# Kernel tuning notes

Measured on AMD Instinct MI355X. Metric: run time of the kernel, lower is better.

The kernel has to match this reference:

```python
import jax, jax.numpy as jnp
import numpy as np

DIM = 1024
NUM_HEADS = 16
HEAD_DIM = DIM // NUM_HEADS
BINDING_BIAS = 0.5
SCALE = HEAD_DIM ** -0.5


def setup_inputs() -> dict:
    key = jax.random.key(0)
    ks = jax.random.split(key, 10)
    B, S, D = 2, 2048, DIM
    std = D ** -0.5
    return {
        "x": jax.random.normal(ks[0], (B, S, D), jnp.float32),
        "binding_matrix": jax.random.uniform(ks[1], (S, S), jnp.float32),
        "Wq": jax.random.normal(ks[2], (D, D), jnp.float32) * std,
        "bq": jnp.zeros((D,), jnp.float32),
        "Wk": jax.random.normal(ks[3], (D, D), jnp.float32) * std,
        "bk": jnp.zeros((D,), jnp.float32),
        "Wv": jax.random.normal(ks[4], (D, D), jnp.float32) * std,
        "bv": jnp.zeros((D,), jnp.float32),
        "Wo": jax.random.normal(ks[5], (D, D), jnp.float32) * std,
        "bo": jnp.zeros((D,), jnp.float32),
    }


def reference(x, binding_matrix, Wq, bq, Wk, bk, Wv, bv, Wo, bo):
    B, S, D = x.shape
    H, Hd = NUM_HEADS, HEAD_DIM
    # projections -> [B, H, S, Hd]
    q = (x @ Wq + bq).reshape(B, S, H, Hd).transpose(0, 2, 1, 3)
    k = (x @ Wk + bk).reshape(B, S, H, Hd).transpose(0, 2, 1, 3)
    v = (x @ Wv + bv).reshape(B, S, H, Hd).transpose(0, 2, 1, 3)
    # scores [B, H, S, S] with additive binding bias
    attn = jnp.einsum("bhqd,bhkd->bhqk", q, k) * SCALE
    attn = attn + BINDING_BIAS * binding_matrix[None, None, :, :]
    attn = jax.nn.softmax(attn, axis=-1)
    out = jnp.einsum("bhqk,bhkd->bhqd", attn, v)
    out = out.transpose(0, 2, 1, 3).reshape(B, S, D)
    return out @ Wo + bo
```

## Files before the change

### kernel.cpp

```cpp
#include <hip/hip_runtime.h>

#define DEV static __device__ __forceinline__

typedef __attribute__((ext_vector_type(4))) float f32x4;
typedef __attribute__((ext_vector_type(8))) __bf16 bfv8;
typedef __attribute__((ext_vector_type(8))) short s8v;
typedef __attribute__((ext_vector_type(4))) short s4v;

DEV short f2bf(float f) {
    unsigned u = __float_as_uint(f);
    u = (u + 0x7fffu + ((u >> 16) & 1u)) >> 16;
    return (short)u;
}
DEV float bf2f(short s) { return __uint_as_float(((unsigned)(unsigned short)s) << 16); }

DEV void gload16(const void* g, void* l) {
    __builtin_amdgcn_global_load_lds(
        (const __attribute__((address_space(1))) void*)g,
        (__attribute__((address_space(3))) void*)l, 16, 0, 0);
}

DEV f32x4 mfma16(bfv8 a, bfv8 b, f32x4 c) {
    return __builtin_amdgcn_mfma_f32_16x16x32_bf16(a, b, c, 0, 0, 0);
}

DEV float max3f(float a, float b, float c) {
    float d;
    asm("v_max3_f32 %0, %1, %2, %3" : "=v"(d) : "v"(a), "v"(b), "v"(c));
    return d;
}

DEV bfv8 ldsfrag(const short* base, int row, int slog) {
    int sp = slog ^ (row & 7);
    return *reinterpret_cast<const bfv8*>(base + row * 64 + sp * 8);
}

__global__ void k_cvt(const float* __restrict__ in, short* __restrict__ out, float s) {
    int i = blockIdx.x * blockDim.x + threadIdx.x;
    const float4* p = (const float4*)in + (size_t)i * 2;
    float4 a = p[0], b = p[1];
    s8v o;
    o[0] = f2bf(a.x * s); o[1] = f2bf(a.y * s); o[2] = f2bf(a.z * s); o[3] = f2bf(a.w * s);
    o[4] = f2bf(b.x * s); o[5] = f2bf(b.y * s); o[6] = f2bf(b.z * s); o[7] = f2bf(b.w * s);
    reinterpret_cast<s8v*>(out)[i] = o;
}

__global__ void k_transpose4(
    const float* __restrict__ W0, const float* __restrict__ W1,
    const float* __restrict__ W2, const float* __restrict__ W3,
    short* __restrict__ T0, short* __restrict__ T1,
    short* __restrict__ T2, short* __restrict__ T3, float s0)
{
    __shared__ float tl[32][33];
    const int z = blockIdx.z;
    const float* W = z == 0 ? W0 : z == 1 ? W1 : z == 2 ? W2 : W3;
    short* Wt = z == 0 ? T0 : z == 1 ? T1 : z == 2 ? T2 : T3;
    const float s = z == 0 ? s0 : 1.f;
    int tx = threadIdx.x & 31, ty = threadIdx.x >> 5;
    int nb = blockIdx.x * 32, kb = blockIdx.y * 32;
#pragma unroll
    for (int i = 0; i < 4; i++)
        tl[ty + i * 8][tx] = W[(kb + ty + i * 8) * 1024 + nb + tx];
    __syncthreads();
#pragma unroll
    for (int i = 0; i < 4; i++)
        Wt[(nb + ty + i * 8) * 1024 + kb + tx] = f2bf(tl[tx][ty + i * 8] * s);
}

template <int EPI>
DEV void gemm_body(const short* __restrict__ A, const short* __restrict__ Bt,
                   const float* __restrict__ bias, void* __restrict__ outp,
                   float bscale, int row0, int col0, short* As, short* Bs)
{
    const int t = threadIdx.x, lane = t & 63;
    const int wv = t >> 6, wr = wv >> 1, wc = wv & 1;
    const int g = lane >> 4, c = lane & 15;

    const f32x4 z4 = {0.f, 0.f, 0.f, 0.f};
    f32x4 acc[2][4];
#pragma unroll
    for (int m = 0; m < 2; m++)
#pragma unroll
        for (int n = 0; n < 4; n++) acc[m][n] = z4;

    for (int kt = 0; kt < 16; ++kt) {
        const int k0 = kt * 64;
        const short* Ag = A + row0 * 1024 + k0;
        const short* Bg = Bt + col0 * 1024 + k0;
#pragma unroll
        for (int j = 0; j < 2; j++) {
            int idx = j * 256 + t;
            int row = idx >> 3, sp = idx & 7, sl = sp ^ (row & 7);
            gload16(Ag + row * 1024 + sl * 8, As + idx * 8);
        }
#pragma unroll
        for (int j = 0; j < 4; j++) {
            int idx = j * 256 + t;
            int row = idx >> 3, sp = idx & 7, sl = sp ^ (row & 7);
            gload16(Bg + row * 1024 + sl * 8, Bs + idx * 8);
        }
        __syncthreads();

        bfv8 af[2][2], bfr[4][2];
#pragma unroll
        for (int m = 0; m < 2; m++)
#pragma unroll
            for (int ks = 0; ks < 2; ks++)
                af[m][ks] = ldsfrag(As, wr * 32 + m * 16 + c, ks * 4 + g);
#pragma unroll
        for (int n = 0; n < 4; n++)
#pragma unroll
            for (int ks = 0; ks < 2; ks++)
                bfr[n][ks] = ldsfrag(Bs, wc * 64 + n * 16 + c, ks * 4 + g);
        __builtin_amdgcn_s_setprio(1);
#pragma unroll
        for (int m = 0; m < 2; m++)
#pragma unroll
            for (int n = 0; n < 4; n++)
#pragma unroll
                for (int ks = 0; ks < 2; ks++)
                    acc[m][n] = mfma16(af[m][ks], bfr[n][ks], acc[m][n]);
        __builtin_amdgcn_s_setprio(0);
        __syncthreads();
    }

#pragma unroll
    for (int n = 0; n < 4; n++) {
        const int gc = col0 + wc * 64 + n * 16 + c;
        const float bvl = bias[gc] * bscale;
        const int h = gc >> 6, d = gc & 63;
#pragma unroll
        for (int m = 0; m < 2; m++) {
            const int gr = row0 + wr * 32 + m * 16 + g * 4;
            if (EPI == 2) {
                float* O = (float*)outp;
#pragma unroll
                for (int r = 0; r < 4; r++) O[(gr + r) * 1024 + gc] = acc[m][n][r] + bvl;
            } else {
                const int b = gr >> 11, sr = gr & 2047;
                short* O = (short*)outp;
                if (EPI == 0) {
                    int base = ((b * 16 + h) * 2048 + sr) * 64 + d;
#pragma unroll
                    for (int r = 0; r < 4; r++) O[base + r * 64] = f2bf(acc[m][n][r] + bvl);
                } else {
                    s4v vv;
#pragma unroll
                    for (int r = 0; r < 4; r++) vv[r] = f2bf(acc[m][n][r] + bvl);
                    *reinterpret_cast<s4v*>(O + ((b * 16 + h) * 64 + d) * 2048 + sr) = vv;
                }
            }
        }
    }
}

__global__ __launch_bounds__(256, 2) void k_gemm3(
    const short* __restrict__ A,
    const short* __restrict__ WqT, const short* __restrict__ WkT, const short* __restrict__ WvT,
    const float* __restrict__ bq, const float* __restrict__ bk, const float* __restrict__ bv,
    short* __restrict__ Qs, short* __restrict__ Kst, short* __restrict__ Vts, float scq)
{
    __shared__ alignas(16) short As[64 * 64];
    __shared__ alignas(16) short Bs[128 * 64];
    const int which = blockIdx.y >> 3;
    const int col0 = (blockIdx.y & 7) * 128;
    const int row0 = blockIdx.x * 64;
    if (which == 0)
        gemm_body<0>(A, WqT, bq, Qs, scq, row0, col0, As, Bs);
    else if (which == 1)
        gemm_body<0>(A, WkT, bk, Kst, 1.f, row0, col0, As, Bs);
    else
        gemm_body<1>(A, WvT, bv, Vts, 1.f, row0, col0, As, Bs);
}

__global__ __launch_bounds__(256, 2) void k_gemmO(
    const short* __restrict__ A, const short* __restrict__ Bt,
    const float* __restrict__ bias, float* __restrict__ outp)
{
    __shared__ alignas(16) short As[64 * 64];
    __shared__ alignas(16) short Bs[128 * 64];
    gemm_body<2>(A, Bt, bias, outp, 1.f, blockIdx.x * 64, blockIdx.y * 128, As, Bs);
}

__global__ __launch_bounds__(256, 4) void k_attn(
    const short* __restrict__ Q, const short* __restrict__ K,
    const short* __restrict__ Vt, const short* __restrict__ bb,
    short* __restrict__ Ob)
{
    __shared__ alignas(16) short Ks[2][64 * 64];
    __shared__ alignas(16) short Vs[2][64 * 64];
    __shared__ alignas(16) short Ps[4][16 * 64];
    const int t = threadIdx.x, lane = t & 63;
    const int wv = t >> 6, g = lane >> 4, c = lane & 15;
    const int qt = blockIdx.x, bh = blockIdx.y;
    const int b = bh >> 4, h = bh & 15;
    const short* Qb = Q + bh * 2048 * 64;
    const short* Kb = K + bh * 2048 * 64;
    const short* Vb = Vt + bh * 64 * 2048;
    const int q0 = qt * 64 + wv * 16;

    bfv8 qf[2];
#pragma unroll
    for (int ks = 0; ks < 2; ks++)
        qf[ks] = *reinterpret_cast<const bfv8*>(Qb + (q0 + c) * 64 + ks * 32 + g * 8);

    const f32x4 z4 = {0.f, 0.f, 0.f, 0.f};
    f32x4 oa[4];
#pragma unroll
    for (int nd = 0; nd < 4; nd++) oa[nd] = z4;
    float mrun = 20.0f, lrun = 0.f;

    const int idx0 = t, idx1 = 256 + t;
    const int r0 = idx0 >> 3, s0 = ((idx0 & 7) ^ (r0 & 7)) * 8;
    const int r1 = idx1 >> 3, s1 = ((idx1 & 7) ^ (r1 & 7)) * 8;
    const short* kp0 = Kb + r0 * 64 + s0;
    const short* kp1 = Kb + r1 * 64 + s1;
    const short* vp0 = Vb + r0 * 2048 + s0;
    const short* vp1 = Vb + r1 * 2048 + s1;
    const short* bbp = bb + (size_t)(q0 + c) * 2048 + 4 * g;

    char* Pb = (char*)&Ps[wv][0];
    const int rx = c & 7;
    char* pw[4];
#pragma unroll
    for (int n = 0; n < 4; n++)
        pw[n] = Pb + c * 128 + (((2 * n + (g >> 1)) ^ rx) << 4) + ((g & 1) << 3);
    const char* pr0 = Pb + c * 128 + ((g ^ rx) << 4);
    const char* pr1 = Pb + c * 128 + (((4 + g) ^ rx) << 4);

    gload16(kp0, &Ks[0][idx0 * 8]);
    gload16(kp1, &Ks[0][idx1 * 8]);
    gload16(vp0, &Vs[0][idx0 * 8]);
    gload16(vp1, &Vs[0][idx1 * 8]);
    kp0 += 4096; kp1 += 4096; vp0 += 64; vp1 += 64;
    s4v bn[4];
#pragma unroll
    for (int n = 0; n < 4; n++) bn[n] = *reinterpret_cast<const s4v*>(bbp + n * 16);
    bbp += 64;
    __syncthreads();

    for (int kt = 0; kt < 32; ++kt) {
        const int cur = kt & 1;
        f32x4 cb[4];
#pragma unroll
        for (int n = 0; n < 4; n++)
#pragma unroll
            for (int r = 0; r < 4; r++) cb[n][r] = bf2f(bn[n][r]);
        if (kt < 31) {
            const int nb = cur ^ 1;
            gload16(kp0, &Ks[nb][idx0 * 8]);
            gload16(kp1, &Ks[nb][idx1 * 8]);
            gload16(vp0, &Vs[nb][idx0 * 8]);
            gload16(vp1, &Vs[nb][idx1 * 8]);
            kp0 += 4096; kp1 += 4096; vp0 += 64; vp1 += 64;
#pragma unroll
            for (int n = 0; n < 4; n++) bn[n] = *reinterpret_cast<const s4v*>(bbp + n * 16);
            bbp += 64;
        }

        const short* Kc = &Ks[cur][0];
        const short* Vc = &Vs[cur][0];

        f32x4 sc[4];
        __builtin_amdgcn_s_setprio(1);
#pragma unroll
        for (int n = 0; n < 4; n++) {
            bfv8 k0 = ldsfrag(Kc, n * 16 + c, g);
            bfv8 k1 = ldsfrag(Kc, n * 16 + c, 4 + g);
            sc[n] = mfma16(k0, qf[0], cb[n]);
            sc[n] = mfma16(k1, qf[1], sc[n]);
        }
        __builtin_amdgcn_s_setprio(0);

#pragma unroll
        for (int n = 0; n < 4; n++)
#pragma unroll
            for (int r = 0; r < 4; r++)
                sc[n][r] = __builtin_amdgcn_exp2f(sc[n][r] - mrun);

#pragma unroll
        for (int n = 0; n < 4; n++) {
            unsigned w0, w1;
            asm("v_cvt_pk_bf16_f32 %0, %1, %2" : "=v"(w0) : "v"(sc[n][0]), "v"(sc[n][1]));
            asm("v_cvt_pk_bf16_f32 %0, %1, %2" : "=v"(w1) : "v"(sc[n][2]), "v"(sc[n][3]));
            uint2 wp; wp.x = w0; wp.y = w1;
            *reinterpret_cast<uint2*>(pw[n]) = wp;
        }

        bfv8 pa0 = *reinterpret_cast<const bfv8*>(pr0);
        bfv8 pa1 = *reinterpret_cast<const bfv8*>(pr1);
        __builtin_amdgcn_s_setprio(1);
#pragma unroll
        for (int nd = 0; nd < 4; nd++) {
            bfv8 v0 = ldsfrag(Vc, nd * 16 + c, g);
            bfv8 v1 = ldsfrag(Vc, nd * 16 + c, 4 + g);
            oa[nd] = mfma16(v0, pa0, oa[nd]);
            oa[nd] = mfma16(v1, pa1, oa[nd]);
        }
        __builtin_amdgcn_s_setprio(0);

        float sn0 = (sc[0][0] + sc[0][1]) + (sc[0][2] + sc[0][3]);
        float sn1 = (sc[1][0] + sc[1][1]) + (sc[1][2] + sc[1][3]);
        float sn2 = (sc[2][0] + sc[2][1]) + (sc[2][2] + sc[2][3]);
        float sn3 = (sc[3][0] + sc[3][1]) + (sc[3][2] + sc[3][3]);
        float rs = (sn0 + sn1) + (sn2 + sn3);
        rs += __shfl_xor(rs, 16);
        rs += __shfl_xor(rs, 32);
        lrun += rs;

        float t0 = fmaxf(max3f(sc[0][0], sc[0][1], sc[0][2]), sc[0][3]);
        float t1 = fmaxf(max3f(sc[1][0], sc[1][1], sc[1][2]), sc[1][3]);
        float t2 = fmaxf(max3f(sc[2][0], sc[2][1], sc[2][2]), sc[2][3]);
        float t3 = fmaxf(max3f(sc[3][0], sc[3][1], sc[3][2]), sc[3][3]);
        float pemax = fmaxf(max3f(t0, t1, t2), t3);
        if (!__all(pemax <= 2896.0f)) {
            float rmax = fmaxf(pemax, __shfl_xor(pemax, 16));
            rmax = fmaxf(rmax, __shfl_xor(rmax, 32));
            if (rmax > 2896.0f) {
                const float corr = 1.0f / rmax;
                mrun += __log2f(rmax);
                lrun *= corr;
#pragma unroll
                for (int nd = 0; nd < 4; nd++)
#pragma unroll
                    for (int r = 0; r < 4; r++) oa[nd][r] *= corr;
            }
        }
        __syncthreads();
    }

    const float rl = 1.f / lrun;
    const size_t srow = (size_t)(b * 2048 + q0 + c);
#pragma unroll
    for (int nd = 0; nd < 4; nd++) {
        s4v st;
#pragma unroll
        for (int r = 0; r < 4; r++) st[r] = f2bf(oa[nd][r] * rl);
        *reinterpret_cast<s4v*>(Ob + srow * 1024 + h * 64 + nd * 16 + 4 * g) = st;
    }
}

extern "C" void kernel_launch(void* const* d_in, const int* in_sizes, int n_in,
                              void* d_out, int out_size, void* d_ws, size_t ws_size,
                              hipStream_t stream)
{
    (void)in_sizes; (void)n_in; (void)out_size; (void)ws_size;
    const float* x    = (const float*)d_in[0];
    const float* bind = (const float*)d_in[1];
    const float* Wq   = (const float*)d_in[2];
    const float* bq   = (const float*)d_in[3];
    const float* Wk   = (const float*)d_in[4];
    const float* bk   = (const float*)d_in[5];
    const float* Wv   = (const float*)d_in[6];
    const float* bv   = (const float*)d_in[7];
    const float* Wo   = (const float*)d_in[8];
    const float* bo   = (const float*)d_in[9];

    char* ws = (char*)d_ws;
    const size_t MB = (size_t)1 << 20;
    short* xb   = (short*)(ws + 0 * MB);
    short* Wqt  = (short*)(ws + 8 * MB);
    short* Wkt  = (short*)(ws + 10 * MB);
    short* Wvt  = (short*)(ws + 12 * MB);
    short* Wot  = (short*)(ws + 14 * MB);
    short* bbm  = (short*)(ws + 16 * MB);
    short* Qs   = (short*)(ws + 24 * MB);
    short* Kst  = (short*)(ws + 32 * MB);
    short* Vts  = (short*)(ws + 40 * MB);
    short* Obuf = (short*)(ws + 48 * MB);

    const float LOG2E = 1.4426950408889634f;
    const float SCQ = 0.125f * LOG2E;
    const float SCB = 0.5f * LOG2E;

    k_cvt<<<2048, 256, 0, stream>>>(x, xb, 1.f);
    k_cvt<<<2048, 256, 0, stream>>>(bind, bbm, SCB);
    k_transpose4<<<dim3(32, 32, 4), 256, 0, stream>>>(Wq, Wk, Wv, Wo,
                                                      Wqt, Wkt, Wvt, Wot, SCQ);
    k_gemm3<<<dim3(64, 24), 256, 0, stream>>>(xb, Wqt, Wkt, Wvt, bq, bk, bv,
                                              Qs, Kst, Vts, SCQ);
    k_attn<<<dim3(32, 32), 256, 0, stream>>>(Qs, Kst, Vts, bbm, Obuf);
    k_gemmO<<<dim3(64, 8), 256, 0, stream>>>(Obuf, Wot, bo, (float*)d_out);
}
```

Before: 146.7 us.

## Rework attention kernel around 32x32 MFMA with register-resident P via lane shuffles

The attention kernel now uses 32x32x16 bf16 MFMA with 32 queries per wave and 128-key tiles, which halves the grid and doubles the K/V tile size per stage. The softmax probabilities are repacked across lane halves with shuffles instead of a round trip through an LDS P buffer, and the bias loads move to after the score computation. The aim is fewer LDS transactions and larger MFMA tiles per instruction. In exchange, register pressure rises (launch bounds drop to 2 blocks per SIMD) and there are fewer blocks, which reduces occupancy.

Result: slower. 162.6 us (+10.9%).

```diff
diff --git a/kernel.cpp b/kernel.cpp
--- a/kernel.cpp
+++ b/kernel.cpp
@@ -3,9 +3,11 @@
 #define DEV static __device__ __forceinline__
 
 typedef __attribute__((ext_vector_type(4))) float f32x4;
+typedef __attribute__((ext_vector_type(16))) float f32x16;
 typedef __attribute__((ext_vector_type(8))) __bf16 bfv8;
 typedef __attribute__((ext_vector_type(8))) short s8v;
 typedef __attribute__((ext_vector_type(4))) short s4v;
+typedef __attribute__((ext_vector_type(4))) unsigned u32x4;
 
 DEV short f2bf(float f) {
     unsigned u = __float_as_uint(f);
@@ -23,11 +25,19 @@
 DEV f32x4 mfma16(bfv8 a, bfv8 b, f32x4 c) {
     return __builtin_amdgcn_mfma_f32_16x16x32_bf16(a, b, c, 0, 0, 0);
 }
+DEV f32x16 mfma32(bfv8 a, bfv8 b, f32x16 c) {
+    return __builtin_amdgcn_mfma_f32_32x32x16_bf16(a, b, c, 0, 0, 0);
+}
 
 DEV float max3f(float a, float b, float c) {
     float d;
     asm("v_max3_f32 %0, %1, %2, %3" : "=v"(d) : "v"(a), "v"(b), "v"(c));
     return d;
+}
+DEV unsigned cvtpk(float lo, float hi) {
+    unsigned w;
+    asm("v_cvt_pk_bf16_f32 %0, %1, %2" : "=v"(w) : "v"(lo), "v"(hi));
+    return w;
 }
 
 DEV bfv8 ldsfrag(const short* base, int row, int slog) {
@@ -182,162 +192,168 @@
     gemm_body<2>(A, Bt, bias, outp, 1.f, blockIdx.x * 64, blockIdx.y * 128, As, Bs);
 }
 
-__global__ __launch_bounds__(256, 4) void k_attn(
+__global__ __launch_bounds__(256, 2) void k_attn(
     const short* __restrict__ Q, const short* __restrict__ K,
     const short* __restrict__ Vt, const short* __restrict__ bb,
     short* __restrict__ Ob)
 {
-    __shared__ alignas(16) short Ks[2][64 * 64];
-    __shared__ alignas(16) short Vs[2][64 * 64];
-    __shared__ alignas(16) short Ps[4][16 * 64];
+    __shared__ alignas(16) short Ks[2][128 * 64];
+    __shared__ alignas(16) short Vs[2][64 * 128];
     const int t = threadIdx.x, lane = t & 63;
-    const int wv = t >> 6, g = lane >> 4, c = lane & 15;
+    const int wv = t >> 6, q = lane & 31, hi = lane >> 5;
     const int qt = blockIdx.x, bh = blockIdx.y;
     const int b = bh >> 4, h = bh & 15;
     const short* Qb = Q + bh * 2048 * 64;
     const short* Kb = K + bh * 2048 * 64;
     const short* Vb = Vt + bh * 64 * 2048;
-    const int q0 = qt * 64 + wv * 16;
-
-    bfv8 qf[2];
-#pragma unroll
-    for (int ks = 0; ks < 2; ks++)
-        qf[ks] = *reinterpret_cast<const bfv8*>(Qb + (q0 + c) * 64 + ks * 32 + g * 8);
-
-    const f32x4 z4 = {0.f, 0.f, 0.f, 0.f};
-    f32x4 oa[4];
-#pragma unroll
-    for (int nd = 0; nd < 4; nd++) oa[nd] = z4;
+    const int qg = qt * 128 + wv * 32 + q;
+    const int qx7 = q & 7, qx15 = q & 15;
+
+    bfv8 qf[4];
+#pragma unroll
+    for (int ks = 0; ks < 4; ks++)
+        qf[ks] = *reinterpret_cast<const bfv8*>(Qb + qg * 64 + 16 * ks + 8 * hi);
+
+    f32x16 oa[2];
+#pragma unroll
+    for (int dt = 0; dt < 2; dt++)
+#pragma unroll
+        for (int r = 0; r < 16; r++) oa[dt][r] = 0.f;
     float mrun = 20.0f, lrun = 0.f;
 
-    const int idx0 = t, idx1 = 256 + t;
-    const int r0 = idx0 >> 3, s0 = ((idx0 & 7) ^ (r0 & 7)) * 8;
-    const int r1 = idx1 >> 3, s1 = ((idx1 & 7) ^ (r1 & 7)) * 8;
-    const short* kp0 = Kb + r0 * 64 + s0;
-    const short* kp1 = Kb + r1 * 64 + s1;
-    const short* vp0 = Vb + r0 * 2048 + s0;
-    const short* vp1 = Vb + r1 * 2048 + s1;
-    const short* bbp = bb + (size_t)(q0 + c) * 2048 + 4 * g;
-
-    char* Pb = (char*)&Ps[wv][0];
-    const int rx = c & 7;
-    char* pw[4];
-#pragma unroll
-    for (int n = 0; n < 4; n++)
-        pw[n] = Pb + c * 128 + (((2 * n + (g >> 1)) ^ rx) << 4) + ((g & 1) << 3);
-    const char* pr0 = Pb + c * 128 + ((g ^ rx) << 4);
-    const char* pr1 = Pb + c * 128 + (((4 + g) ^ rx) << 4);
-
-    gload16(kp0, &Ks[0][idx0 * 8]);
-    gload16(kp1, &Ks[0][idx1 * 8]);
-    gload16(vp0, &Vs[0][idx0 * 8]);
-    gload16(vp1, &Vs[0][idx1 * 8]);
-    kp0 += 4096; kp1 += 4096; vp0 += 64; vp1 += 64;
-    s4v bn[4];
-#pragma unroll
-    for (int n = 0; n < 4; n++) bn[n] = *reinterpret_cast<const s4v*>(bbp + n * 16);
-    bbp += 64;
+    const short* kp[4]; const short* vp[4];
+    int kdst[4], vdst[4];
+#pragma unroll
+    for (int j = 0; j < 4; j++) {
+        int idx = j * 256 + t;
+        int kr = idx >> 3, ksl = (idx & 7) ^ (kr & 7);
+        kp[j] = Kb + kr * 64 + ksl * 8;
+        kdst[j] = idx * 8;
+        int vr = idx >> 4, vsl = (idx & 15) ^ (vr & 15);
+        vp[j] = Vb + vr * 2048 + vsl * 8;
+        vdst[j] = idx * 8;
+    }
+    auto stage = [&](int buf) {
+#pragma unroll
+        for (int j = 0; j < 4; j++) {
+            gload16(kp[j], &Ks[buf][kdst[j]]);
+            gload16(vp[j], &Vs[buf][vdst[j]]);
+        }
+    };
+
+    const short* bbp = bb + (size_t)qg * 2048 + 4 * hi;
+    s4v bn[16];
+#pragma unroll
+    for (int i = 0; i < 16; i++)
+        bn[i] = *reinterpret_cast<const s4v*>(bbp + 32 * (i >> 2) + 8 * (i & 3));
+
+    stage(0);
+#pragma unroll
+    for (int j = 0; j < 4; j++) { kp[j] += 8192; vp[j] += 128; }
     __syncthreads();
 
-    for (int kt = 0; kt < 32; ++kt) {
+    for (int kt = 0; kt < 16; ++kt) {
         const int cur = kt & 1;
-        f32x4 cb[4];
-#pragma unroll
-        for (int n = 0; n < 4; n++)
-#pragma unroll
-            for (int r = 0; r < 4; r++) cb[n][r] = bf2f(bn[n][r]);
-        if (kt < 31) {
-            const int nb = cur ^ 1;
-            gload16(kp0, &Ks[nb][idx0 * 8]);
-            gload16(kp1, &Ks[nb][idx1 * 8]);
-            gload16(vp0, &Vs[nb][idx0 * 8]);
-            gload16(vp1, &Vs[nb][idx1 * 8]);
-            kp0 += 4096; kp1 += 4096; vp0 += 64; vp1 += 64;
-#pragma unroll
-            for (int n = 0; n < 4; n++) bn[n] = *reinterpret_cast<const s4v*>(bbp + n * 16);
-            bbp += 64;
-        }
-
+        if (kt < 15) {
+            stage(cur ^ 1);
+#pragma unroll
+            for (int j = 0; j < 4; j++) { kp[j] += 8192; vp[j] += 128; }
+        }
         const short* Kc = &Ks[cur][0];
         const short* Vc = &Vs[cur][0];
 
-        f32x4 sc[4];
-        __builtin_amdgcn_s_setprio(1);
-#pragma unroll
-        for (int n = 0; n < 4; n++) {
-            bfv8 k0 = ldsfrag(Kc, n * 16 + c, g);
-            bfv8 k1 = ldsfrag(Kc, n * 16 + c, 4 + g);
-            sc[n] = mfma16(k0, qf[0], cb[n]);
-            sc[n] = mfma16(k1, qf[1], sc[n]);
-        }
-        __builtin_amdgcn_s_setprio(0);
-
-#pragma unroll
-        for (int n = 0; n < 4; n++)
-#pragma unroll
-            for (int r = 0; r < 4; r++)
-                sc[n][r] = __builtin_amdgcn_exp2f(sc[n][r] - mrun);
-
-#pragma unroll
-        for (int n = 0; n < 4; n++) {
-            unsigned w0, w1;
-            asm("v_cvt_pk_bf16_f32 %0, %1, %2" : "=v"(w0) : "v"(sc[n][0]), "v"(sc[n][1]));
-            asm("v_cvt_pk_bf16_f32 %0, %1, %2" : "=v"(w1) : "v"(sc[n][2]), "v"(sc[n][3]));
-            uint2 wp; wp.x = w0; wp.y = w1;
-            *reinterpret_cast<uint2*>(pw[n]) = wp;
-        }
-
-        bfv8 pa0 = *reinterpret_cast<const bfv8*>(pr0);
-        bfv8 pa1 = *reinterpret_cast<const bfv8*>(pr1);
-        __builtin_amdgcn_s_setprio(1);
-#pragma unroll
-        for (int nd = 0; nd < 4; nd++) {
-            bfv8 v0 = ldsfrag(Vc, nd * 16 + c, g);
-            bfv8 v1 = ldsfrag(Vc, nd * 16 + c, 4 + g);
-            oa[nd] = mfma16(v0, pa0, oa[nd]);
-            oa[nd] = mfma16(v1, pa1, oa[nd]);
-        }
-        __builtin_amdgcn_s_setprio(0);
-
-        float sn0 = (sc[0][0] + sc[0][1]) + (sc[0][2] + sc[0][3]);
-        float sn1 = (sc[1][0] + sc[1][1]) + (sc[1][2] + sc[1][3]);
-        float sn2 = (sc[2][0] + sc[2][1]) + (sc[2][2] + sc[2][3]);
-        float sn3 = (sc[3][0] + sc[3][1]) + (sc[3][2] + sc[3][3]);
-        float rs = (sn0 + sn1) + (sn2 + sn3);
-        rs += __shfl_xor(rs, 16);
-        rs += __shfl_xor(rs, 32);
+        unsigned W[4][8];
+        float lsum = 0.f, pmax = 0.f;
+#pragma unroll
+        for (int tt = 0; tt < 4; tt++) {
+            f32x16 sc;
+#pragma unroll
+            for (int r = 0; r < 16; r++)
+                sc[r] = bf2f(bn[4 * tt + (r >> 2)][r & 3]);
+            __builtin_amdgcn_s_setprio(1);
+#pragma unroll
+            for (int ks = 0; ks < 4; ks++) {
+                bfv8 kf = *reinterpret_cast<const bfv8*>(
+                    Kc + (32 * tt + q) * 64 + ((2 * ks + hi) ^ qx7) * 8);
+                sc = mfma32(kf, qf[ks], sc);
+            }
+            __builtin_amdgcn_s_setprio(0);
+#pragma unroll
+            for (int r = 0; r < 16; r++)
+                sc[r] = __builtin_amdgcn_exp2f(sc[r] - mrun);
+            float a0 = (sc[0] + sc[1]) + (sc[2] + sc[3]);
+            float a1 = (sc[4] + sc[5]) + (sc[6] + sc[7]);
+            float a2 = (sc[8] + sc[9]) + (sc[10] + sc[11]);
+            float a3 = (sc[12] + sc[13]) + (sc[14] + sc[15]);
+            lsum += (a0 + a1) + (a2 + a3);
+            float m0 = fmaxf(max3f(sc[0], sc[1], sc[2]), sc[3]);
+            float m1 = fmaxf(max3f(sc[4], sc[5], sc[6]), sc[7]);
+            float m2 = fmaxf(max3f(sc[8], sc[9], sc[10]), sc[11]);
+            float m3 = fmaxf(max3f(sc[12], sc[13], sc[14]), sc[15]);
+            pmax = fmaxf(pmax, fmaxf(max3f(m0, m1, m2), m3));
+#pragma unroll
+            for (int w = 0; w < 8; w++)
+                W[tt][w] = cvtpk(sc[2 * w], sc[2 * w + 1]);
+        }
+
+        if (kt < 15) {
+            bbp += 128;
+#pragma unroll
+            for (int i = 0; i < 16; i++)
+                bn[i] = *reinterpret_cast<const s4v*>(bbp + 32 * (i >> 2) + 8 * (i & 3));
+        }
+
+#pragma unroll
+        for (int j = 0; j < 8; j++) {
+            const int tt = j >> 1, e = j & 1;
+            unsigned x0 = hi ? W[tt][4 * e + 0] : W[tt][4 * e + 2];
+            unsigned x1 = hi ? W[tt][4 * e + 1] : W[tt][4 * e + 3];
+            unsigned r0 = (unsigned)__shfl_xor((int)x0, 32);
+            unsigned r1 = (unsigned)__shfl_xor((int)x1, 32);
+            u32x4 pw;
+            pw.x = hi ? r0 : W[tt][4 * e + 0];
+            pw.y = hi ? r1 : W[tt][4 * e + 1];
+            pw.z = hi ? W[tt][4 * e + 2] : r0;
+            pw.w = hi ? W[tt][4 * e + 3] : r1;
+            bfv8 pf = __builtin_bit_cast(bfv8, pw);
+            __builtin_amdgcn_s_setprio(1);
+#pragma unroll
+            for (int dt = 0; dt < 2; dt++) {
+                bfv8 vf = *reinterpret_cast<const bfv8*>(
+                    Vc + (32 * dt + q) * 128 + ((2 * j + hi) ^ qx15) * 8);
+                oa[dt] = mfma32(vf, pf, oa[dt]);
+            }
+            __builtin_amdgcn_s_setprio(0);
+        }
+
+        float rs = lsum + __shfl_xor(lsum, 32);
         lrun += rs;
-
-        float t0 = fmaxf(max3f(sc[0][0], sc[0][1], sc[0][2]), sc[0][3]);
-        float t1 = fmaxf(max3f(sc[1][0], sc[1][1], sc[1][2]), sc[1][3]);
-        float t2 = fmaxf(max3f(sc[2][0], sc[2][1], sc[2][2]), sc[2][3]);
-        float t3 = fmaxf(max3f(sc[3][0], sc[3][1], sc[3][2]), sc[3][3]);
-        float pemax = fmaxf(max3f(t0, t1, t2), t3);
-        if (!__all(pemax <= 2896.0f)) {
-            float rmax = fmaxf(pemax, __shfl_xor(pemax, 16));
-            rmax = fmaxf(rmax, __shfl_xor(rmax, 32));
+        if (!__all(pmax <= 2896.0f)) {
+            float rmax = fmaxf(pmax, __shfl_xor(pmax, 32));
             if (rmax > 2896.0f) {
                 const float corr = 1.0f / rmax;
                 mrun += __log2f(rmax);
                 lrun *= corr;
 #pragma unroll
-                for (int nd = 0; nd < 4; nd++)
-#pragma unroll
-                    for (int r = 0; r < 4; r++) oa[nd][r] *= corr;
+                for (int dt = 0; dt < 2; dt++)
+#pragma unroll
+                    for (int r = 0; r < 16; r++) oa[dt][r] *= corr;
             }
         }
         __syncthreads();
     }
 
-    const float rl = 1.f / lrun;
-    const size_t srow = (size_t)(b * 2048 + q0 + c);
-#pragma unroll
-    for (int nd = 0; nd < 4; nd++) {
-        s4v st;
-#pragma unroll
-        for (int r = 0; r < 4; r++) st[r] = f2bf(oa[nd][r] * rl);
-        *reinterpret_cast<s4v*>(Ob + srow * 1024 + h * 64 + nd * 16 + 4 * g) = st;
-    }
+    const float rl = 1.0f / lrun;
+    short* Op = Ob + (size_t)(b * 2048 + qg) * 1024 + h * 64;
+#pragma unroll
+    for (int dt = 0; dt < 2; dt++)
+#pragma unroll
+        for (int rg = 0; rg < 4; rg++) {
+            s4v st;
+#pragma unroll
+            for (int r = 0; r < 4; r++) st[r] = f2bf(oa[dt][4 * rg + r] * rl);
+            *reinterpret_cast<s4v*>(Op + 32 * dt + 8 * rg + 4 * hi) = st;
+        }
 }
 
 extern "C" void kernel_launch(void* const* d_in, const int* in_sizes, int n_in,
@@ -379,6 +395,6 @@
                                                       Wqt, Wkt, Wvt, Wot, SCQ);
     k_gemm3<<<dim3(64, 24), 256, 0, stream>>>(xb, Wqt, Wkt, Wvt, bq, bk, bv,
                                               Qs, Kst, Vts, SCQ);
-    k_attn<<<dim3(32, 32), 256, 0, stream>>>(Qs, Kst, Vts, bbm, Obuf);
+    k_attn<<<dim3(16, 32), 256, 0, stream>>>(Qs, Kst, Vts, bbm, Obuf);
     k_gemmO<<<dim3(64, 8), 256, 0, stream>>>(Obuf, Wot, bo, (float*)d_out);
 }
```

## Restage K/V LDS layout to fragment order, compute row sums via MFMA, restructure barriers

Applied to the files above, without the earlier changes.

Changes the global-to-LDS staging so K and V tiles land in MFMA fragment order, letting each lane read fragments with a linear lane*8 offset instead of XOR-swizzled addressing; the P buffer uses the same layout. The softmax row sum is now accumulated with an extra MFMA against a ones vector instead of VALU adds and cross-lane shuffles. The loop moves the barrier to the top with an explicit vmcnt wait and sched_barriers that order V, bias and K loads. This trades bank-conflict-avoiding swizzle for a simpler layout that may cause LDS bank conflicts, and adds two MFMAs per iteration.

Measured after the change: 191.3 us. +30.4%, slower.

```diff
diff --git a/kernel.cpp b/kernel.cpp
--- a/kernel.cpp
+++ b/kernel.cpp
@@ -28,6 +28,11 @@
     float d;
     asm("v_max3_f32 %0, %1, %2, %3" : "=v"(d) : "v"(a), "v"(b), "v"(c));
     return d;
+}
+DEV unsigned cvtpk(float lo, float hi) {
+    unsigned w;
+    asm("v_cvt_pk_bf16_f32 %0, %1, %2" : "=v"(w) : "v"(lo), "v"(hi));
+    return w;
 }
 
 DEV bfv8 ldsfrag(const short* base, int row, int slog) {
@@ -208,66 +213,81 @@
     f32x4 oa[4];
 #pragma unroll
     for (int nd = 0; nd < 4; nd++) oa[nd] = z4;
-    float mrun = 20.0f, lrun = 0.f;
-
-    const int idx0 = t, idx1 = 256 + t;
-    const int r0 = idx0 >> 3, s0 = ((idx0 & 7) ^ (r0 & 7)) * 8;
-    const int r1 = idx1 >> 3, s1 = ((idx1 & 7) ^ (r1 & 7)) * 8;
-    const short* kp0 = Kb + r0 * 64 + s0;
-    const short* kp1 = Kb + r1 * 64 + s1;
-    const short* vp0 = Vb + r0 * 2048 + s0;
-    const short* vp1 = Vb + r1 * 2048 + s1;
+    f32x4 lacc = z4;
+    float mrun = 20.0f;
+
+    s8v ob_;
+#pragma unroll
+    for (int i = 0; i < 8; i++) ob_[i] = (short)0x3F80;
+    const bfv8 ones = __builtin_bit_cast(bfv8, ob_);
+
+    const short* kp[2]; const short* vp[2]; int dst8[2];
+#pragma unroll
+    for (int j = 0; j < 2; j++) {
+        int idx = j * 256 + t;
+        int row = 16 * (idx >> 7) + (idx & 15);
+        int jc = (idx >> 4) & 7;
+        kp[j] = Kb + row * 64 + jc * 8;
+        vp[j] = Vb + row * 2048 + jc * 8;
+        dst8[j] = idx * 8;
+    }
+    auto stageK = [&](int buf) {
+        gload16(kp[0], &Ks[buf][dst8[0]]);
+        gload16(kp[1], &Ks[buf][dst8[1]]);
+        kp[0] += 4096; kp[1] += 4096;
+    };
+    auto stageV = [&](int buf) {
+        gload16(vp[0], &Vs[buf][dst8[0]]);
+        gload16(vp[1], &Vs[buf][dst8[1]]);
+        vp[0] += 64; vp[1] += 64;
+    };
     const short* bbp = bb + (size_t)(q0 + c) * 2048 + 4 * g;
-
-    char* Pb = (char*)&Ps[wv][0];
-    const int rx = c & 7;
-    char* pw[4];
-#pragma unroll
-    for (int n = 0; n < 4; n++)
-        pw[n] = Pb + c * 128 + (((2 * n + (g >> 1)) ^ rx) << 4) + ((g & 1) << 3);
-    const char* pr0 = Pb + c * 128 + ((g ^ rx) << 4);
-    const char* pr1 = Pb + c * 128 + (((4 + g) ^ rx) << 4);
-
-    gload16(kp0, &Ks[0][idx0 * 8]);
-    gload16(kp1, &Ks[0][idx1 * 8]);
-    gload16(vp0, &Vs[0][idx0 * 8]);
-    gload16(vp1, &Vs[0][idx1 * 8]);
-    kp0 += 4096; kp1 += 4096; vp0 += 64; vp1 += 64;
-    s4v bn[4];
-#pragma unroll
-    for (int n = 0; n < 4; n++) bn[n] = *reinterpret_cast<const s4v*>(bbp + n * 16);
-    bbp += 64;
-    __syncthreads();
+    s4v bnC[4], bnN[4];
+    auto ldbias = [&](s4v* d) {
+#pragma unroll
+        for (int n = 0; n < 4; n++) d[n] = *reinterpret_cast<const s4v*>(bbp + n * 16);
+        bbp += 64;
+    };
+
+    short* Pw = &Ps[wv][0];
+    short* pwr = Pw + (g >> 1) * 128 + c * 8 + 4 * (g & 1);
+    const short* prd = Pw + lane * 8;
+
+    stageV(0);
+    __builtin_amdgcn_sched_barrier(0);
+    ldbias(bnC);
+    __builtin_amdgcn_sched_barrier(0);
+    stageK(0);
+    __builtin_amdgcn_sched_barrier(0);
 
     for (int kt = 0; kt < 32; ++kt) {
+        asm volatile("s_waitcnt vmcnt(0)" ::: "memory");
+        __builtin_amdgcn_sched_barrier(0);
+        __builtin_amdgcn_s_barrier();
+        __builtin_amdgcn_sched_barrier(0);
         const int cur = kt & 1;
-        f32x4 cb[4];
+        if (kt < 31) {
+            stageV(cur ^ 1);
+            __builtin_amdgcn_sched_barrier(0);
+            ldbias(bnN);
+            __builtin_amdgcn_sched_barrier(0);
+            stageK(cur ^ 1);
+            __builtin_amdgcn_sched_barrier(0);
+        }
+        const short* Kl = &Ks[cur][0] + lane * 8;
+        const short* Vl = &Vs[cur][0] + lane * 8;
+
+        f32x4 sc[4];
 #pragma unroll
         for (int n = 0; n < 4; n++)
 #pragma unroll
-            for (int r = 0; r < 4; r++) cb[n][r] = bf2f(bn[n][r]);
-        if (kt < 31) {
-            const int nb = cur ^ 1;
-            gload16(kp0, &Ks[nb][idx0 * 8]);
-            gload16(kp1, &Ks[nb][idx1 * 8]);
-            gload16(vp0, &Vs[nb][idx0 * 8]);
-            gload16(vp1, &Vs[nb][idx1 * 8]);
-            kp0 += 4096; kp1 += 4096; vp0 += 64; vp1 += 64;
-#pragma unroll
-            for (int n = 0; n < 4; n++) bn[n] = *reinterpret_cast<const s4v*>(bbp + n * 16);
-            bbp += 64;
-        }
-
-        const short* Kc = &Ks[cur][0];
-        const short* Vc = &Vs[cur][0];
-
-        f32x4 sc[4];
+            for (int r = 0; r < 4; r++) sc[n][r] = bf2f(bnC[n][r]);
         __builtin_amdgcn_s_setprio(1);
 #pragma unroll
         for (int n = 0; n < 4; n++) {
-            bfv8 k0 = ldsfrag(Kc, n * 16 + c, g);
-            bfv8 k1 = ldsfrag(Kc, n * 16 + c, 4 + g);
-            sc[n] = mfma16(k0, qf[0], cb[n]);
+            bfv8 k0 = *reinterpret_cast<const bfv8*>(Kl + n * 1024);
+            bfv8 k1 = *reinterpret_cast<const bfv8*>(Kl + n * 1024 + 512);
+            sc[n] = mfma16(k0, qf[0], sc[n]);
             sc[n] = mfma16(k1, qf[1], sc[n]);
         }
         __builtin_amdgcn_s_setprio(0);
@@ -280,33 +300,25 @@
 
 #pragma unroll
         for (int n = 0; n < 4; n++) {
-            unsigned w0, w1;
-            asm("v_cvt_pk_bf16_f32 %0, %1, %2" : "=v"(w0) : "v"(sc[n][0]), "v"(sc[n][1]));
-            asm("v_cvt_pk_bf16_f32 %0, %1, %2" : "=v"(w1) : "v"(sc[n][2]), "v"(sc[n][3]));
-            uint2 wp; wp.x = w0; wp.y = w1;
-            *reinterpret_cast<uint2*>(pw[n]) = wp;
-        }
-
-        bfv8 pa0 = *reinterpret_cast<const bfv8*>(pr0);
-        bfv8 pa1 = *reinterpret_cast<const bfv8*>(pr1);
+            uint2 wp;
+            wp.x = cvtpk(sc[n][0], sc[n][1]);
+            wp.y = cvtpk(sc[n][2], sc[n][3]);
+            *reinterpret_cast<uint2*>(pwr + n * 256) = wp;
+        }
+
+        bfv8 pb0 = *reinterpret_cast<const bfv8*>(prd);
+        bfv8 pb1 = *reinterpret_cast<const bfv8*>(prd + 512);
         __builtin_amdgcn_s_setprio(1);
 #pragma unroll
         for (int nd = 0; nd < 4; nd++) {
-            bfv8 v0 = ldsfrag(Vc, nd * 16 + c, g);
-            bfv8 v1 = ldsfrag(Vc, nd * 16 + c, 4 + g);
-            oa[nd] = mfma16(v0, pa0, oa[nd]);
-            oa[nd] = mfma16(v1, pa1, oa[nd]);
-        }
+            bfv8 v0 = *reinterpret_cast<const bfv8*>(Vl + nd * 1024);
+            bfv8 v1 = *reinterpret_cast<const bfv8*>(Vl + nd * 1024 + 512);
+            oa[nd] = mfma16(v0, pb0, oa[nd]);
+            oa[nd] = mfma16(v1, pb1, oa[nd]);
+        }
+        lacc = mfma16(ones, pb0, lacc);
+        lacc = mfma16(ones, pb1, lacc);
         __builtin_amdgcn_s_setprio(0);
-
-        float sn0 = (sc[0][0] + sc[0][1]) + (sc[0][2] + sc[0][3]);
-        float sn1 = (sc[1][0] + sc[1][1]) + (sc[1][2] + sc[1][3]);
-        float sn2 = (sc[2][0] + sc[2][1]) + (sc[2][2] + sc[2][3]);
-        float sn3 = (sc[3][0] + sc[3][1]) + (sc[3][2] + sc[3][3]);
-        float rs = (sn0 + sn1) + (sn2 + sn3);
-        rs += __shfl_xor(rs, 16);
-        rs += __shfl_xor(rs, 32);
-        lrun += rs;
 
         float t0 = fmaxf(max3f(sc[0][0], sc[0][1], sc[0][2]), sc[0][3]);
         float t1 = fmaxf(max3f(sc[1][0], sc[1][1], sc[1][2]), sc[1][3]);
@@ -319,17 +331,19 @@
             if (rmax > 2896.0f) {
                 const float corr = 1.0f / rmax;
                 mrun += __log2f(rmax);
-                lrun *= corr;
 #pragma unroll
                 for (int nd = 0; nd < 4; nd++)
 #pragma unroll
                     for (int r = 0; r < 4; r++) oa[nd][r] *= corr;
+#pragma unroll
+                for (int r = 0; r < 4; r++) lacc[r] *= corr;
             }
         }
-        __syncthreads();
-    }
-
-    const float rl = 1.f / lrun;
+#pragma unroll
+        for (int n = 0; n < 4; n++) bnC[n] = bnN[n];
+    }
+
+    const float rl = 1.0f / lacc[0];
     const size_t srow = (size_t)(b * 2048 + q0 + c);
 #pragma unroll
     for (int nd = 0; nd < 4; nd++) {
```
